# Kernel optimization log

Measured on AMD Instinct MI355X. Metric: run time of the kernel, lower is better.

Reference implementation:

```python
import jax, jax.numpy as jnp
import numpy as np

NUM_HEADS = 16
EPS = 1e-12  # softmax_2relu eps
MASK_VALUE = -1e9  # stands in for torch.finfo(dtype).min; relu zeroes it anyway


def setup_inputs() -> dict:
    key = jax.random.key(0)
    k1, k2, k3 = jax.random.split(key, 3)
    B, S, D = 4, 1024, 1024
    hidden_states = jax.random.normal(k1, (B, S, D), dtype=jnp.float32)
    c_attn_w = jax.random.normal(k2, (D, 3 * D), dtype=jnp.float32) * 0.02
    c_attn_b = jnp.zeros((3 * D,), dtype=jnp.float32)
    c_proj_w = jax.random.normal(k3, (D, D), dtype=jnp.float32) * 0.02
    c_proj_b = jnp.zeros((D,), dtype=jnp.float32)
    return {
        "hidden_states": hidden_states,
        "c_attn_w": c_attn_w,
        "c_attn_b": c_attn_b,
        "c_proj_w": c_proj_w,
        "c_proj_b": c_proj_b,
    }


def softmax_2relu(scores, axis=-1, eps=EPS):
    r = jax.nn.relu(scores)
    n = scores.shape[axis]
    return (r + eps / n) / (jnp.sum(r, axis=axis, keepdims=True) + eps)


def reference(hidden_states, c_attn_w, c_attn_b, c_proj_w, c_proj_b):
    B, S, D = hidden_states.shape
    H = NUM_HEADS
    dh = D // H

    # fused QKV projection (Conv1D: x @ W + b)
    qkv = hidden_states @ c_attn_w + c_attn_b  # [B, S, 3D]
    q, k, v = jnp.split(qkv, 3, axis=-1)

    def to_heads(t):
        return t.reshape(B, S, H, dh).transpose(0, 2, 1, 3)  # [B, H, S, dh]

    q, k, v = to_heads(q), to_heads(k), to_heads(v)

    # attention scores, scaled
    scores = jnp.einsum("bhqd,bhkd->bhqk", q, k) / jnp.sqrt(
        jnp.asarray(dh, dtype=hidden_states.dtype)
    )

    # causal mask: masked positions set to large negative (relu -> 0)
    causal = jnp.tril(jnp.ones((S, S), dtype=bool))
    scores = jnp.where(causal[None, None, :, :], scores, MASK_VALUE)

    # custom relu-softmax normalization (softmax_2relu)
    attn = softmax_2relu(scores, axis=-1)

    ctx = jnp.einsum("bhqk,bhkd->bhqd", attn, v)  # [B, H, S, dh]
    ctx = ctx.transpose(0, 2, 1, 3).reshape(B, S, D)

    out = ctx @ c_proj_w + c_proj_b
    return out
```

## Files before the change

### kernel.cpp

```cpp
#include <hip/hip_runtime.h>
#include <hip/hip_bf16.h>

typedef unsigned short u16;
typedef unsigned int u32;

#define AS1 __attribute__((address_space(1)))
#define AS3 __attribute__((address_space(3)))

typedef __attribute__((ext_vector_type(8))) __bf16 bf16x8;
typedef __attribute__((ext_vector_type(4))) float f32x4;
typedef __attribute__((ext_vector_type(8))) u16 u16x8;

static __device__ __forceinline__ u16 f2bf(float f) {
    u32 x = __builtin_bit_cast(u32, f);
    u32 r = (x + 0x7fffu + ((x >> 16) & 1u)) >> 16;
    return (u16)r;
}
static __device__ __forceinline__ float bf2f(u16 u) {
    u32 x = ((u32)u) << 16;
    return __builtin_bit_cast(float, x);
}
static __device__ __forceinline__ void gload_lds16(const void* g, void* l) {
    __builtin_amdgcn_global_load_lds((const AS1 u32*)g, (AS3 u32*)l, 16, 0, 0);
}
static __device__ __forceinline__ u32 cvtpk(float lo, float hi) {
    u32 r;
    asm("v_cvt_pk_bf16_f32 %0, %1, %2" : "=v"(r) : "v"(lo), "v"(hi));
    return r;
}

__global__ __launch_bounds__(256) void k_cast_bf16(const float* __restrict__ in,
                                                   u16* __restrict__ out, int n8) {
    int i = blockIdx.x * 256 + threadIdx.x;
    if (i >= n8) return;
    typedef __attribute__((ext_vector_type(4))) float fx4;
    const fx4* p = (const fx4*)in;
    fx4 a = p[2 * i], b = p[2 * i + 1];
    u16x8 o;
    o[0] = f2bf(a[0]); o[1] = f2bf(a[1]); o[2] = f2bf(a[2]); o[3] = f2bf(a[3]);
    o[4] = f2bf(b[0]); o[5] = f2bf(b[1]); o[6] = f2bf(b[2]); o[7] = f2bf(b[3]);
    *(u16x8*)(out + (size_t)i * 8) = o;
}

__global__ __launch_bounds__(256) void k_wtrans(const float* __restrict__ W,
                                                u16* __restrict__ Wt, int K_, int N_) {
    __shared__ u16 T[64][65];
    int nt = blockIdx.x, kt = blockIdx.y;
    int t = threadIdx.x, c = t & 63, r0 = t >> 6;
#pragma unroll
    for (int i = 0; i < 16; i++) {
        int k = r0 + i * 4;
        T[k][c] = f2bf(W[(size_t)(kt * 64 + k) * N_ + nt * 64 + c]);
    }
    __syncthreads();
#pragma unroll
    for (int i = 0; i < 16; i++) {
        int nn = r0 + i * 4;
        Wt[(size_t)(nt * 64 + nn) * K_ + kt * 64 + c] = T[c][nn];
    }
}

template <int EPI>
__global__ __launch_bounds__(256, 2) void k_gemm(
    const u16* __restrict__ A, const u16* __restrict__ Bt,
    const float* __restrict__ bias, float* __restrict__ outf,
    u16* __restrict__ Qb, u16* __restrict__ Kb, u16* __restrict__ Vb,
    int Msz, int Nsz, int Ksz) {
    __shared__ u16 Al[128 * 64];
    __shared__ u16 Bl[128 * 64];
    int tid = threadIdx.x;
    int m0 = blockIdx.x * 128, n0 = blockIdx.y * 128;
    int w = tid >> 6, lane = tid & 63, l15 = lane & 15, lg = lane >> 4;
    int wr = (w >> 1) * 64, wc = (w & 1) * 64;
    f32x4 acc[4][4] = {};

    for (int k0 = 0; k0 < Ksz; k0 += 64) {
#pragma unroll
        for (int i = 0; i < 4; i++) {
            int c = i * 256 + tid;
            gload_lds16(A + (size_t)(m0 + (c >> 3)) * Ksz + k0 + (c & 7) * 8,
                        &Al[(c & ~63) * 8]);
        }
#pragma unroll
        for (int i = 0; i < 4; i++) {
            int c = i * 256 + tid;
            gload_lds16(Bt + (size_t)(n0 + (c >> 3)) * Ksz + k0 + (c & 7) * 8,
                        &Bl[(c & ~63) * 8]);
        }
        __syncthreads();
#pragma unroll
        for (int kk = 0; kk < 2; kk++) {
            bf16x8 af[4], bfr[4];
#pragma unroll
            for (int m = 0; m < 4; m++)
                af[m] = *(const bf16x8*)&Al[(wr + m * 16 + l15) * 64 + kk * 32 + lg * 8];
#pragma unroll
            for (int n = 0; n < 4; n++)
                bfr[n] = *(const bf16x8*)&Bl[(wc + n * 16 + l15) * 64 + kk * 32 + lg * 8];
#pragma unroll
            for (int m = 0; m < 4; m++)
#pragma unroll
                for (int n = 0; n < 4; n++)
                    acc[m][n] = __builtin_amdgcn_mfma_f32_16x16x32_bf16(af[m], bfr[n], acc[m][n], 0, 0, 0);
        }
        __syncthreads();
    }

    if (EPI == 0) {
#pragma unroll
        for (int n = 0; n < 4; n++) {
            int gn = n0 + wc + n * 16 + l15;
            float bv = bias[gn];
#pragma unroll
            for (int m = 0; m < 4; m++) {
                int gmb = m0 + wr + m * 16 + lg * 4;
#pragma unroll
                for (int r = 0; r < 4; r++)
                    outf[(size_t)(gmb + r) * Nsz + gn] = acc[m][n][r] + bv;
            }
        }
    } else {
#pragma unroll
        for (int n = 0; n < 4; n++) {
            int gn = n0 + wc + n * 16 + l15;
            float bv = bias[gn];
            int which = gn >> 10, d = gn & 1023, h = d >> 6, dd = d & 63;
            u16* dst = which == 0 ? Qb : (which == 1 ? Kb : Vb);
#pragma unroll
            for (int m = 0; m < 4; m++) {
                int gmb = m0 + wr + m * 16 + lg * 4;
#pragma unroll
                for (int r = 0; r < 4; r++) {
                    int gm = gmb + r;
                    int b = gm >> 10, s = gm & 1023;
                    dst[((size_t)(b * 16 + h) * 1024 + s) * 64 + dd] = f2bf(acc[m][n][r] + bv);
                }
            }
        }
    }
}

__global__ __launch_bounds__(256) void k_vtrans(const u16* __restrict__ Vb,
                                                u16* __restrict__ Vt,
                                                float* __restrict__ vpart) {
    __shared__ u16 T[64][65];
    __shared__ float red[4][64];
    int st = blockIdx.x, bh = blockIdx.y;
    int t = threadIdx.x, c = t & 63, r0 = t >> 6;
    const u16* Vh = Vb + (size_t)bh * 65536;
    u16* Vth = Vt + (size_t)bh * 65536;
    float a = 0.f;
#pragma unroll
    for (int i = 0; i < 16; i++) {
        int s = r0 + i * 4;
        u16 v = Vh[(size_t)(st * 64 + s) * 64 + c];
        T[s][c] = v;
        a += bf2f(v);
    }
    red[r0][c] = a;
    __syncthreads();
#pragma unroll
    for (int i = 0; i < 16; i++) {
        int d = r0 + i * 4;
        Vth[(size_t)d * 1024 + st * 64 + c] = T[c][d];
    }
    if (r0 == 0)
        vpart[((size_t)bh * 16 + st) * 64 + c] =
            red[0][c] + red[1][c] + red[2][c] + red[3][c];
}

__global__ __launch_bounds__(256) void k_vsum2(const float* __restrict__ vpart,
                                               float* __restrict__ vsum) {
    int idx = blockIdx.x * 256 + threadIdx.x;
    int bh = idx >> 6, d = idx & 63;
    const float* p = vpart + (size_t)bh * 1024 + d;
    float s = 0.f;
#pragma unroll
    for (int st = 0; st < 16; st++) s += p[st * 64];
    vsum[idx] = s;
}

__global__ __launch_bounds__(512, 4) void k_attn(const u16* __restrict__ Qb,
                                                 const u16* __restrict__ Kb,
                                                 const u16* __restrict__ Vt,
                                                 const float* __restrict__ vsum,
                                                 u16* __restrict__ ctx) {
    __shared__ u16 Kl[2][4096];
    __shared__ u16 Vl[2][4096];
    __shared__ u16 Pl[8 * 1024];
    __shared__ float rsw[8][16];
    int tid = threadIdx.x, w = tid >> 6, lane = tid & 63, l15 = lane & 15, lg = lane >> 4;
    int p = blockIdx.x;
    int tb = 7 - (p >> 6);
    int bh = p & 63;
    int qb = tb * 128 + w * 16;
    int nkb = 2 * tb + 2;
    int klast = (qb + 15) >> 6;

    const u16* Qh = Qb + (size_t)bh * 65536;
    const u16* Kh = Kb + (size_t)bh * 65536;
    const u16* Vh = Vt + (size_t)bh * 65536;
    u16* Pw = &Pl[w * 1024];
    int swz = (l15 & 7) << 4;
    int q = qb + l15;

    bf16x8 qf[2];
#pragma unroll
    for (int kk = 0; kk < 2; kk++)
        qf[kk] = *(const bf16x8*)(Qh + (size_t)q * 64 + kk * 32 + lg * 8);
    float vs[4];
#pragma unroll
    for (int n = 0; n < 4; n++) vs[n] = vsum[bh * 64 + n * 16 + l15];

    int srow = tid >> 3, schunk = tid & 7;
    int soff = ((schunk * 16) ^ ((srow & 7) << 4)) >> 1;
    u16* kdst = &Kl[0][0] + w * 512;
    u16* vdst = &Vl[0][0] + w * 512;

    f32x4 ctxa[4] = {};
    float rsp = 0.f;
    int cur = 0;

    gload_lds16(Kh + (size_t)srow * 64 + soff, kdst);
    gload_lds16(Vh + (size_t)srow * 1024 + soff, vdst);
    __syncthreads();

    for (int kb = 0; kb < nkb; kb++) {
        if (kb + 1 < nkb) {
            int nx = cur ^ 1;
            gload_lds16(Kh + (size_t)(((kb + 1) << 6) + srow) * 64 + soff,
                        &Kl[nx][0] + w * 512);
            gload_lds16(Vh + (size_t)srow * 1024 + ((kb + 1) << 6) + soff,
                        &Vl[nx][0] + w * 512);
        }
        if (kb <= klast) {
            bool masked = (kb == klast);
            const char* Kc = (const char*)&Kl[cur][0];
            const char* Vc = (const char*)&Vl[cur][0];
            f32x4 sc[4] = {};
#pragma unroll
            for (int kk = 0; kk < 2; kk++)
#pragma unroll
                for (int n = 0; n < 4; n++) {
                    bf16x8 kf = *(const bf16x8*)(Kc + ((((n * 16 + l15) << 7) + (kk << 6) + (lg << 4)) ^ swz));
                    sc[n] = __builtin_amdgcn_mfma_f32_16x16x32_bf16(kf, qf[kk], sc[n], 0, 0, 0);
                }
            int qml = q - (kb << 6) - (lg << 2);
#pragma unroll
            for (int n = 0; n < 4; n++) {
                float v0 = fmaxf(sc[n][0] * 0.125f, 0.f);
                float v1 = fmaxf(sc[n][1] * 0.125f, 0.f);
                float v2 = fmaxf(sc[n][2] * 0.125f, 0.f);
                float v3 = fmaxf(sc[n][3] * 0.125f, 0.f);
                if (masked) {
                    int c = qml - n * 16;
                    v0 = (0 <= c) ? v0 : 0.f;
                    v1 = (1 <= c) ? v1 : 0.f;
                    v2 = (2 <= c) ? v2 : 0.f;
                    v3 = (3 <= c) ? v3 : 0.f;
                }
                rsp += (v0 + v1) + (v2 + v3);
                u32 w0 = cvtpk(v0, v1), w1 = cvtpk(v2, v3);
                int base = l15 * 128 + n * 32 + lg * 8;
                *(u32*)((char*)Pw + ((base) ^ swz)) = w0;
                *(u32*)((char*)Pw + ((base + 4) ^ swz)) = w1;
            }
            bf16x8 pf0 = *(const bf16x8*)((char*)Pw + ((l15 * 128 + lg * 16) ^ swz));
            bf16x8 pf1 = *(const bf16x8*)((char*)Pw + ((l15 * 128 + 64 + lg * 16) ^ swz));
#pragma unroll
            for (int n = 0; n < 4; n++) {
                bf16x8 vf = *(const bf16x8*)(Vc + ((((n * 16 + l15) << 7) + (lg << 4)) ^ swz));
                ctxa[n] = __builtin_amdgcn_mfma_f32_16x16x32_bf16(pf0, vf, ctxa[n], 0, 0, 0);
            }
#pragma unroll
            for (int n = 0; n < 4; n++) {
                bf16x8 vf = *(const bf16x8*)(Vc + ((((n * 16 + l15) << 7) + 64 + (lg << 4)) ^ swz));
                ctxa[n] = __builtin_amdgcn_mfma_f32_16x16x32_bf16(pf1, vf, ctxa[n], 0, 0, 0);
            }
        }
        __syncthreads();
        cur ^= 1;
    }

    float tsum = rsp;
    tsum += __shfl_xor(tsum, 16);
    tsum += __shfl_xor(tsum, 32);
    rsw[w][l15] = tsum;
    f32x4 rv = *(f32x4*)&rsw[w][lg * 4];
    const float EPS = 1e-12f, EPSN = 1e-12f / 1024.f;
    float inv[4];
#pragma unroll
    for (int r = 0; r < 4; r++) inv[r] = 1.f / (rv[r] + EPS);
    int b = bh >> 4, h = bh & 15;
#pragma unroll
    for (int n = 0; n < 4; n++) {
#pragma unroll
        for (int r = 0; r < 4; r++) {
            int qq = qb + lg * 4 + r;
            float val = (ctxa[n][r] + EPSN * vs[n]) * inv[r];
            ctx[(size_t)(b * 1024 + qq) * 1024 + h * 64 + n * 16 + l15] = f2bf(val);
        }
    }
}

__global__ __launch_bounds__(256) void k_qkfix(const float* __restrict__ X,
                                               const float* __restrict__ W,
                                               const float* __restrict__ bias,
                                               float* __restrict__ Qf,
                                               float* __restrict__ Kf) {
    __shared__ float red[4][8][64];
    int cb = blockIdx.x;
    int b = blockIdx.y >> 1, rh = blockIdx.y & 1;
    int tid = threadIdx.x, w = tid >> 6, lane = tid & 63;
    int col = cb * 64 + lane;

    const float* Wp = W + (size_t)(w * 256) * 3072 + col;
    const float* Xp = X + ((size_t)b * 1024 + rh * 8) * 1024 + w * 256;
    float acc[8] = {};
#pragma unroll 8
    for (int it = 0; it < 256; ++it) {
        float wv = Wp[(size_t)it * 3072];
#pragma unroll
        for (int j = 0; j < 8; j++) acc[j] += Xp[(size_t)j * 1024 + it] * wv;
    }
#pragma unroll
    for (int j = 0; j < 8; j++) red[w][j][lane] = acc[j];
    __syncthreads();

    int isK = cb >> 4, h = cb & 15;
    float* dst = isK ? Kf : Qf;
#pragma unroll
    for (int o = tid; o < 512; o += 256) {
        int j = o >> 6, c = o & 63;
        float s = red[0][j][c] + red[1][j][c] + red[2][j][c] + red[3][j][c];
        dst[((size_t)(b * 16 + h) * 16 + rh * 8 + j) * 64 + c] = s + bias[cb * 64 + c];
    }
}

__global__ __launch_bounds__(256) void k_attnfix(const float* __restrict__ Qf,
                                                 const float* __restrict__ Kf,
                                                 const u16* __restrict__ Vb,
                                                 const float* __restrict__ vsum,
                                                 u16* __restrict__ ctx) {
    __shared__ float ps[16][17];
    __shared__ float dens[16];
    int bh = blockIdx.x, t = threadIdx.x;
    int q = t >> 4, k = t & 15;
    const float* Qr = Qf + ((size_t)bh * 16 + q) * 64;
    const float* Kr = Kf + ((size_t)bh * 16 + k) * 64;
    float s = 0.f;
    for (int d = 0; d < 64; d++) s += Qr[d] * Kr[d];
    s *= 0.125f;
    float p = (k <= q) ? fmaxf(s, 0.f) : 0.f;
    float den = p;
    den += __shfl_xor(den, 1); den += __shfl_xor(den, 2);
    den += __shfl_xor(den, 4); den += __shfl_xor(den, 8);
    ps[q][k] = p;
    if (k == 0) dens[q] = den;
    __syncthreads();
    int d0 = (t & 15) * 4;
    float c[4] = {};
    for (int kk = 0; kk <= q; kk++) {
        float pv = ps[q][kk];
        const u16* vr = Vb + ((size_t)bh * 1024 + kk) * 64 + d0;
        c[0] += pv * bf2f(vr[0]); c[1] += pv * bf2f(vr[1]);
        c[2] += pv * bf2f(vr[2]); c[3] += pv * bf2f(vr[3]);
    }
    float inv = 1.f / (dens[q] + 1e-12f);
    const float EPSN = 1e-12f / 1024.f;
    const float* vs = vsum + bh * 64 + d0;
    int b = bh >> 4, h = bh & 15;
    u16* dst = ctx + (size_t)(b * 1024 + q) * 1024 + h * 64 + d0;
#pragma unroll
    for (int j = 0; j < 4; j++) dst[j] = f2bf((c[j] + EPSN * vs[j]) * inv);
}

extern "C" void kernel_launch(void* const* d_in, const int* in_sizes, int n_in,
                              void* d_out, int out_size, void* d_ws, size_t ws_size,
                              hipStream_t stream) {
    const float* X = (const float*)d_in[0];
    const float* Wqkv = (const float*)d_in[1];
    const float* bqkv = (const float*)d_in[2];
    const float* Wproj = (const float*)d_in[3];
    const float* bproj = (const float*)d_in[4];
    float* out = (float*)d_out;
    char* ws = (char*)d_ws;

    u16* Xb     = (u16*)(ws);
    u16* Wqkvt  = (u16*)(ws + 8388608);
    u16* Wprojt = (u16*)(ws + 14680064);
    u16* Qb     = (u16*)(ws + 16777216);
    u16* Kb     = (u16*)(ws + 25165824);
    u16* Vb     = (u16*)(ws + 33554432);
    u16* Vt     = (u16*)(ws + 41943040);
    float* vsum = (float*)(ws + 50331648);
    float* Qf   = (float*)(ws + 50348032);
    float* Kf   = (float*)(ws + 50610176);
    float* vpart= (float*)(ws + 50872320);
    u16* ctx    = Xb;

    k_cast_bf16<<<dim3(2048), dim3(256), 0, stream>>>(X, Xb, 524288);
    k_wtrans<<<dim3(48, 16), dim3(256), 0, stream>>>(Wqkv, Wqkvt, 1024, 3072);
    k_wtrans<<<dim3(16, 16), dim3(256), 0, stream>>>(Wproj, Wprojt, 1024, 1024);
    k_gemm<1><<<dim3(32, 24), dim3(256), 0, stream>>>(Xb, Wqkvt, bqkv, nullptr,
                                                      Qb, Kb, Vb, 4096, 3072, 1024);
    k_vtrans<<<dim3(16, 64), dim3(256), 0, stream>>>(Vb, Vt, vpart);
    k_vsum2<<<dim3(16), dim3(256), 0, stream>>>(vpart, vsum);
    k_qkfix<<<dim3(32, 8), dim3(256), 0, stream>>>(X, Wqkv, bqkv, Qf, Kf);
    k_attn<<<dim3(512), dim3(512), 0, stream>>>(Qb, Kb, Vt, vsum, ctx);
    k_attnfix<<<dim3(64), dim3(256), 0, stream>>>(Qf, Kf, Vb, vsum, ctx);
    k_gemm<0><<<dim3(32, 8), dim3(256), 0, stream>>>(ctx, Wprojt, bproj, out,
                                                     nullptr, nullptr, nullptr, 4096, 1024, 1024);
}
```

Before: 136.5 us.

## Replace QKV GEMM with 256x256-tile, 8-wave, 4-stage pipelined kernel

Adds a new QKV projection GEMM that uses 256x256 output tiles with 512 threads, a 4-slot LDS ring filled by direct global-to-LDS loads, swizzled LDS reads, and interleaved half-tile MFMA phases with priority boosts and explicit vmcnt waits. Blocks are remapped so neighbouring tiles land on the same XCD group. The aim is more data reuse per byte loaded and better overlap of memory traffic with MFMA work than the old 128x128 kernel. The risks are fewer blocks (192) for the CU count, higher register pressure, and a hand-unrolled schedule that hardcodes K=1024.

```diff
diff --git a/kernel.cpp b/kernel.cpp
--- a/kernel.cpp
+++ b/kernel.cpp
@@ -59,6 +59,131 @@
         Wt[(size_t)(nt * 64 + nn) * K_ + kt * 64 + c] = T[c][nn];
     }
 }
+
+__global__ __launch_bounds__(512, 2) void k_gemm8(
+    const u16* __restrict__ A, const u16* __restrict__ Bt,
+    const float* __restrict__ bias,
+    u16* __restrict__ Qb, u16* __restrict__ Kb, u16* __restrict__ Vb,
+    int Nsz, int Ksz) {
+    __shared__ __align__(16) u16 Asl[4 * 8192];
+    __shared__ __align__(16) u16 Bsl[4 * 8192];
+    int tid = threadIdx.x, w = tid >> 6, lane = tid & 63;
+    int l15 = lane & 15, lg = lane >> 4;
+    int wm = w >> 2, wn = w & 3;
+    int bid = blockIdx.x;
+    int cpx = gridDim.x >> 3;
+    int logi = (bid & 7) * cpx + (bid >> 3);
+    int ntiles = Nsz >> 8;
+    int mt = logi / ntiles, nt = logi % ntiles;
+    int m0 = mt << 8, n0 = nt << 8;
+
+    int scol = ((lane & 3) << 3) ^ (((lane >> 5) & 1) << 4);
+    int rswz = (l15 & 8) << 2;
+    int srow = (w << 4) + (lane >> 2);
+
+    f32x4 acc[8][4] = {};
+    bf16x8 af[8], bf[2];
+
+    auto stageA = [&](int tt, int kk) {
+        u16* base = Asl + (((2 * tt + kk) & 3) << 13) + (w << 9);
+        const u16* s0 = A + (size_t)(m0 + srow) * Ksz + (tt << 6) + (kk << 5) + scol;
+        gload_lds16(s0, base);
+        gload_lds16(s0 + (size_t)128 * Ksz, base + 4096);
+    };
+    auto stageB = [&](int tt, int kk) {
+        u16* base = Bsl + (((2 * tt + kk) & 3) << 13) + (w << 9);
+        const u16* s0 = Bt + (size_t)(n0 + srow) * Ksz + (tt << 6) + (kk << 5) + scol;
+        gload_lds16(s0, base);
+        gload_lds16(s0 + (size_t)128 * Ksz, base + 4096);
+    };
+    auto loadA = [&](int slot) {
+#pragma unroll
+        for (int m = 0; m < 8; m++) {
+            int row = (wm << 7) + (m << 4) + l15;
+            af[m] = *(const bf16x8*)((const char*)Asl + (slot << 14) + row * 64 + ((lg << 4) ^ rswz));
+        }
+    };
+    auto loadB = [&](int slot, int nh) {
+#pragma unroll
+        for (int nn = 0; nn < 2; nn++) {
+            int row = (wn << 6) + ((nh * 2 + nn) << 4) + l15;
+            bf[nn] = *(const bf16x8*)((const char*)Bsl + (slot << 14) + row * 64 + ((lg << 4) ^ rswz));
+        }
+    };
+    auto mfma0 = [&]() {
+        __builtin_amdgcn_s_setprio(1);
+#pragma unroll
+        for (int m = 0; m < 8; m++) {
+            acc[m][0] = __builtin_amdgcn_mfma_f32_16x16x32_bf16(af[m], bf[0], acc[m][0], 0, 0, 0);
+            acc[m][1] = __builtin_amdgcn_mfma_f32_16x16x32_bf16(af[m], bf[1], acc[m][1], 0, 0, 0);
+        }
+        __builtin_amdgcn_s_setprio(0);
+    };
+    auto mfma1 = [&]() {
+        __builtin_amdgcn_s_setprio(1);
+#pragma unroll
+        for (int m = 0; m < 8; m++) {
+            acc[m][2] = __builtin_amdgcn_mfma_f32_16x16x32_bf16(af[m], bf[0], acc[m][2], 0, 0, 0);
+            acc[m][3] = __builtin_amdgcn_mfma_f32_16x16x32_bf16(af[m], bf[1], acc[m][3], 0, 0, 0);
+        }
+        __builtin_amdgcn_s_setprio(0);
+    };
+#define BAR_() { __builtin_amdgcn_s_barrier(); asm volatile("" ::: "memory"); }
+#define VMW(n) asm volatile("s_waitcnt vmcnt(" #n ")" ::: "memory")
+
+    stageA(0, 0); stageB(0, 0); stageA(0, 1); stageB(0, 1); stageA(1, 0); stageB(1, 0);
+    VMW(8);
+    BAR_();
+
+#pragma unroll 1
+    for (int t = 0; t < 14; t++) {
+        int s0 = (2 * t) & 3, s1 = (2 * t + 1) & 3;
+        loadA(s0); loadB(s0, 0); stageA(t + 1, 1);
+        BAR_(); mfma0(); BAR_();
+        loadB(s0, 1); stageB(t + 1, 1);
+        BAR_(); mfma1(); VMW(8); BAR_();
+        loadA(s1); loadB(s1, 0); stageA(t + 2, 0);
+        BAR_(); mfma0(); BAR_();
+        loadB(s1, 1); stageB(t + 2, 0);
+        BAR_(); mfma1(); VMW(8); BAR_();
+    }
+    loadA(0); loadB(0, 0); stageA(15, 1);
+    BAR_(); mfma0(); BAR_();
+    loadB(0, 1); stageB(15, 1);
+    BAR_(); mfma1(); VMW(8); BAR_();
+    loadA(1); loadB(1, 0);
+    BAR_(); mfma0(); BAR_();
+    loadB(1, 1);
+    BAR_(); mfma1(); VMW(4); BAR_();
+    loadA(2); loadB(2, 0);
+    BAR_(); mfma0(); BAR_();
+    loadB(2, 1);
+    BAR_(); mfma1(); VMW(0); BAR_();
+    loadA(3); loadB(3, 0);
+    BAR_(); mfma0(); BAR_();
+    loadB(3, 1);
+    BAR_(); mfma1(); BAR_();
+
+#pragma unroll
+    for (int n = 0; n < 4; n++) {
+        int gn = n0 + (wn << 6) + (n << 4) + l15;
+        float bv = bias[gn];
+        int which = gn >> 10, d = gn & 1023, h = d >> 6, dd = d & 63;
+        u16* dst = which == 0 ? Qb : (which == 1 ? Kb : Vb);
+#pragma unroll
+        for (int m = 0; m < 8; m++) {
+            int gmb = m0 + (wm << 7) + (m << 4) + (lg << 2);
+#pragma unroll
+            for (int r = 0; r < 4; r++) {
+                int gm = gmb + r;
+                int b = gm >> 10, s = gm & 1023;
+                dst[((size_t)(b * 16 + h) * 1024 + s) * 64 + dd] = f2bf(acc[m][n][r] + bv);
+            }
+        }
+    }
+}
+#undef BAR_
+#undef VMW
 
 template <int EPI>
 __global__ __launch_bounds__(256, 2) void k_gemm(
@@ -402,8 +527,7 @@
     k_cast_bf16<<<dim3(2048), dim3(256), 0, stream>>>(X, Xb, 524288);
     k_wtrans<<<dim3(48, 16), dim3(256), 0, stream>>>(Wqkv, Wqkvt, 1024, 3072);
     k_wtrans<<<dim3(16, 16), dim3(256), 0, stream>>>(Wproj, Wprojt, 1024, 1024);
-    k_gemm<1><<<dim3(32, 24), dim3(256), 0, stream>>>(Xb, Wqkvt, bqkv, nullptr,
-                                                      Qb, Kb, Vb, 4096, 3072, 1024);
+    k_gemm8<<<dim3(192), dim3(512), 0, stream>>>(Xb, Wqkvt, bqkv, Qb, Kb, Vb, 3072, 1024);
     k_vtrans<<<dim3(16, 64), dim3(256), 0, stream>>>(Vb, Vt, vpart);
     k_vsum2<<<dim3(16), dim3(256), 0, stream>>>(vpart, vsum);
     k_qkfix<<<dim3(32, 8), dim3(256), 0, stream>>>(X, Wqkv, bqkv, Qf, Kf);
```

Result: no change. 138.3 us (+1.4%).
